# Kernel optimization log

Measured on AMD Instinct MI355X. Metric: run time of the kernel, lower is better.

Reference implementation:

```python
import jax, jax.numpy as jnp
import numpy as np
from jax import lax

DN = ('NCHW', 'OIHW', 'NCHW')


def setup_inputs() -> dict:
    key = jax.random.key(0)
    ks = jax.random.split(key, 5)
    B, C, H, W = 1, 128, 64, 64
    heads = 4
    return {
        'x_q': jax.random.normal(ks[0], (B, C, H, W), jnp.float32),
        'x_kv': jax.random.normal(ks[1], (B, C, H, W), jnp.float32),
        'w_qkv': jax.random.normal(ks[2], (3 * C, C, 1, 1), jnp.float32) * 0.05,
        'w_dw': jax.random.normal(ks[3], (3 * C, 1, 3, 3), jnp.float32) * 0.2,
        'w_proj': jax.random.normal(ks[4], (C, C, 1, 1), jnp.float32) * 0.05,
        'temperature': jnp.ones((heads, 1, 1), jnp.float32),
    }


def reference(x_q, x_kv, w_qkv, w_dw, w_proj, temperature):
    B, C, H, W = x_q.shape
    heads = temperature.shape[0]
    hd = C // heads
    N = H * W

    # shared qkv 1x1 conv + depthwise 3x3 conv on concatenated [2B,C,H,W]
    x = jnp.concatenate([x_q, x_kv], axis=0)
    qkv = lax.conv_general_dilated(x, w_qkv, (1, 1), 'VALID', dimension_numbers=DN)
    qkv = lax.conv_general_dilated(qkv, w_dw, (1, 1), 'SAME',
                                   feature_group_count=3 * C, dimension_numbers=DN)
    q, k, v = jnp.split(qkv, 3, axis=1)
    q = q[:B]          # query branch from x_q
    k = k[B:]          # key/value branch from x_kv
    v = v[B:]

    def to_heads(t):   # [B,C,H,W] -> [B,h,N,d]
        return t.reshape(B, heads, hd, N).transpose(0, 1, 3, 2)

    attn = jnp.einsum('bhnd,bhmd->bhnm', to_heads(q), to_heads(k)) * temperature
    attn = jax.nn.softmax(attn, axis=-1)
    out = jnp.einsum('bhnm,bhmd->bhnd', attn, to_heads(v))
    out = out.transpose(0, 1, 3, 2).reshape(B, C, H, W)
    return lax.conv_general_dilated(out, w_proj, (1, 1), 'VALID', dimension_numbers=DN)
```

## Files before the change

### kernel.cpp

```cpp
#include <hip/hip_runtime.h>

typedef short bf16x4 __attribute__((ext_vector_type(4)));
typedef short bf16x8 __attribute__((ext_vector_type(8)));
typedef float f32x4 __attribute__((ext_vector_type(4)));
typedef unsigned short u16x4 __attribute__((ext_vector_type(4)));
typedef unsigned short u16x8 __attribute__((ext_vector_type(8)));

__device__ __forceinline__ unsigned short f2bf(float f) {
  union { float f; unsigned u; } v; v.f = f;
  unsigned r = v.u + 0x7FFFu + ((v.u >> 16) & 1u);
  return (unsigned short)(r >> 16);
}
__device__ __forceinline__ unsigned fbits(float f) {
  union { float f; unsigned u; } x; x.f = f; return x.u;
}
__device__ __forceinline__ float bfloat(unsigned u) {
  union { unsigned u; float f; } x; x.u = u; return x.f;
}
__device__ __forceinline__ float fexp2(float x) {
#if __has_builtin(__builtin_amdgcn_exp2f)
  return __builtin_amdgcn_exp2f(x);
#else
  return exp2f(x);
#endif
}
__device__ __forceinline__ f32x4 pv_mfma(bf16x4 a, bf16x4 b, f32x4 c) {
#if __has_builtin(__builtin_amdgcn_mfma_f32_16x16x16bf16_1k)
  return __builtin_amdgcn_mfma_f32_16x16x16bf16_1k(a, b, c, 0, 0, 0);
#else
  bf16x8 az = {a[0], a[1], a[2], a[3], 0, 0, 0, 0};
  bf16x8 bz = {b[0], b[1], b[2], b[3], 0, 0, 0, 0};
  return __builtin_amdgcn_mfma_f32_16x16x32_bf16(az, bz, c, 0, 0, 0);
#endif
}

__global__ __launch_bounds__(256)
void cast_kernel(const float* __restrict__ Xq, const float* __restrict__ Xkv,
                 const float* __restrict__ Wqkv, const float* __restrict__ Wproj,
                 unsigned short* __restrict__ XT, unsigned short* __restrict__ Wq16,
                 unsigned short* __restrict__ Wph, unsigned short* __restrict__ Wpl)
{
  const int b = blockIdx.x, t = threadIdx.x;
  if (b < 256) {
    __shared__ __align__(16) float Tl[64][68];
    const int img = b >> 7, kt = (b >> 6) & 1, nt = b & 63;
    const float* X = img ? Xkv : Xq;
    #pragma unroll
    for (int i = 0; i < 4; ++i) {
      int e = i * 256 + t;
      int r = e >> 4, c4 = (e & 15) * 4;
      *(f32x4*)&Tl[r][c4] = *(const f32x4*)&X[(kt * 64 + r) * 4096 + nt * 64 + c4];
    }
    __syncthreads();
    unsigned short* out = XT + img * (4096 * 128);
    #pragma unroll
    for (int i = 0; i < 2; ++i) {
      int u = i * 256 + t;
      int n = u >> 3, kg = u & 7;
      u16x8 tv;
      #pragma unroll
      for (int j = 0; j < 8; ++j) tv[j] = f2bf(Tl[kg * 8 + j][n]);
      *(u16x8*)&out[(nt * 64 + n) * 128 + kt * 64 + kg * 8] = tv;
    }
  } else {
    const int wb = b - 256;
    if (wb < 3) {
      #pragma unroll 4
      for (int i = 0; i < 64; ++i) {
        int idx = wb * 16384 + i * 256 + t;
        Wq16[idx] = f2bf(Wqkv[idx]);
      }
    } else {
      #pragma unroll 4
      for (int i = 0; i < 64; ++i) {
        int idx = i * 256 + t;
        float v = Wproj[idx];
        unsigned short h = f2bf(v);
        float hf = bfloat((unsigned)h << 16);
        Wph[idx] = h;
        Wpl[idx] = f2bf(v - hf);
      }
    }
  }
}

__global__ __launch_bounds__(256)
void gemm_qkv_kernel(const unsigned short* __restrict__ XT,
                     const unsigned short* __restrict__ Wq16,
                     unsigned short* __restrict__ Y16)
{
  const int t = threadIdx.x;
  const int w = t >> 6, c = t & 15, g = (t & 63) >> 4;
  const int n0 = blockIdx.x * 32;
  const int ob = blockIdx.y;
  const int o_base = ob * 64 + w * 16;
  const unsigned short* B = XT + (ob >= 2 ? 4096 * 128 : 0);
  f32x4 acc0 = {0.f, 0.f, 0.f, 0.f}, acc1 = {0.f, 0.f, 0.f, 0.f};
  #pragma unroll
  for (int ks = 0; ks < 4; ++ks) {
    bf16x8 a = *(const bf16x8*)&Wq16[(o_base + c) * 128 + ks * 32 + g * 8];
    bf16x8 b0 = *(const bf16x8*)&B[(n0 + c) * 128 + ks * 32 + g * 8];
    bf16x8 b1 = *(const bf16x8*)&B[(n0 + 16 + c) * 128 + ks * 32 + g * 8];
    acc0 = __builtin_amdgcn_mfma_f32_16x16x32_bf16(a, b0, acc0, 0, 0, 0);
    acc1 = __builtin_amdgcn_mfma_f32_16x16x32_bf16(a, b1, acc1, 0, 0, 0);
  }
  #pragma unroll
  for (int i = 0; i < 4; ++i) {
    Y16[(o_base + 4 * g + i) * 4096 + n0 + c] = f2bf(acc0[i]);
    Y16[(o_base + 4 * g + i) * 4096 + n0 + 16 + c] = f2bf(acc1[i]);
  }
}

__global__ __launch_bounds__(256)
void gemm_proj_kernel(const unsigned short* __restrict__ Oth,
                      const unsigned short* __restrict__ Otl,
                      const unsigned short* __restrict__ Wph,
                      const unsigned short* __restrict__ Wpl, float* __restrict__ Y)
{
  const int t = threadIdx.x;
  const int w = t >> 6, c = t & 15, g = (t & 63) >> 4;
  const int n0 = blockIdx.x * 32;
  const int o_base = blockIdx.y * 64 + w * 16;
  f32x4 acc0 = {0.f, 0.f, 0.f, 0.f}, acc1 = {0.f, 0.f, 0.f, 0.f};
  #pragma unroll
  for (int ks = 0; ks < 4; ++ks) {
    const int ko = ks * 32 + g * 8;
    bf16x8 ah = *(const bf16x8*)&Wph[(o_base + c) * 128 + ko];
    bf16x8 al = *(const bf16x8*)&Wpl[(o_base + c) * 128 + ko];
    bf16x8 bh0 = *(const bf16x8*)&Oth[(n0 + c) * 128 + ko];
    bf16x8 bl0 = *(const bf16x8*)&Otl[(n0 + c) * 128 + ko];
    bf16x8 bh1 = *(const bf16x8*)&Oth[(n0 + 16 + c) * 128 + ko];
    bf16x8 bl1 = *(const bf16x8*)&Otl[(n0 + 16 + c) * 128 + ko];
    acc0 = __builtin_amdgcn_mfma_f32_16x16x32_bf16(al, bh0, acc0, 0, 0, 0);
    acc0 = __builtin_amdgcn_mfma_f32_16x16x32_bf16(ah, bl0, acc0, 0, 0, 0);
    acc0 = __builtin_amdgcn_mfma_f32_16x16x32_bf16(ah, bh0, acc0, 0, 0, 0);
    acc1 = __builtin_amdgcn_mfma_f32_16x16x32_bf16(al, bh1, acc1, 0, 0, 0);
    acc1 = __builtin_amdgcn_mfma_f32_16x16x32_bf16(ah, bl1, acc1, 0, 0, 0);
    acc1 = __builtin_amdgcn_mfma_f32_16x16x32_bf16(ah, bh1, acc1, 0, 0, 0);
  }
  #pragma unroll
  for (int i = 0; i < 4; ++i) {
    Y[(o_base + 4 * g + i) * 4096 + n0 + c] = acc0[i];
    Y[(o_base + 4 * g + i) * 4096 + n0 + 16 + c] = acc1[i];
  }
}

__global__ __launch_bounds__(256)
void dwconv_kernel(const unsigned short* __restrict__ T16, const float* __restrict__ Wd,
                   const float* __restrict__ temp, unsigned short* __restrict__ Qb)
{
  __shared__ __align__(16) float P[4096];
  const int jc = blockIdx.x;
  const int t = threadIdx.x;
  const unsigned short* in = T16 + jc * 4096;
  #pragma unroll
  for (int i = 0; i < 2; ++i) {
    u16x8 v = *(const u16x8*)&in[(i * 256 + t) * 8];
    #pragma unroll
    for (int j = 0; j < 8; ++j)
      P[(i * 256 + t) * 8 + j] = bfloat((unsigned)v[j] << 16);
  }
  float w[9];
  #pragma unroll
  for (int k = 0; k < 9; ++k) w[k] = Wd[jc * 9 + k];
  const float scale = (jc < 128) ? temp[jc >> 5] * 1.4426950408889634f : 1.0f;
  __syncthreads();
  unsigned short* out = Qb + jc * 4096;
  #pragma unroll 4
  for (int i = 0; i < 16; ++i) {
    int idx = i * 256 + t;
    int y = idx >> 6, x = idx & 63;
    float acc = 0.f;
    #pragma unroll
    for (int dy = -1; dy <= 1; ++dy) {
      int yy = y + dy;
      if (yy < 0 || yy > 63) continue;
      #pragma unroll
      for (int dx = -1; dx <= 1; ++dx) {
        int xx = x + dx;
        if (xx < 0 || xx > 63) continue;
        acc += w[(dy + 1) * 3 + (dx + 1)] * P[yy * 64 + xx];
      }
    }
    out[idx] = f2bf(acc * scale);
  }
}

#define KOFF (128 * 4096)
#define VOFF (256 * 4096)

__global__ __launch_bounds__(1024, 4)
void attn_kernel(const unsigned short* __restrict__ Qb,
                 unsigned short* __restrict__ Oth, unsigned short* __restrict__ Otl)
{
  __shared__ __align__(16) char lds[40960];
  const int t = threadIdx.x;
  const int wv = t >> 6;
  const int g4 = wv >> 2, qw = wv & 3;
  const int l = t & 63;
  const int c = l & 15, g = l >> 4;
  const int h = blockIdx.y;
  const int nq = blockIdx.x * 64;
  const int m0w = wv * 256;

  bf16x8 qf[4];
  #pragma unroll
  for (int s = 0; s < 4; ++s)
    #pragma unroll
    for (int e = 0; e < 8; ++e)
      qf[s][e] = (short)Qb[(h * 32 + g * 8 + e) * 4096 + nq + s * 16 + c];

  f32x4 oh[4][2];
  #pragma unroll
  for (int s = 0; s < 4; ++s) {
    oh[s][0] = (f32x4){0.f, 0.f, 0.f, 0.f};
    oh[s][1] = (f32x4){0.f, 0.f, 0.f, 0.f};
  }
  float lsum[4] = {0.f, 0.f, 0.f, 0.f};

  const unsigned short* Kb = Qb + KOFF + (h * 32 + g * 8) * 4096 + m0w + c;
  const unsigned short* Vb0 = Qb + VOFF + (h * 32 + c) * 4096 + m0w + g * 4;
  const unsigned short* Vb1 = Vb0 + 16 * 4096;

  #pragma unroll 4
  for (int j = 0; j < 16; ++j) {
    bf16x8 kf;
    #pragma unroll
    for (int e = 0; e < 8; ++e)
      kf[e] = (short)Kb[e * 4096 + j * 16];
    bf16x4 vf0 = *(const bf16x4*)&Vb0[j * 16];
    bf16x4 vf1 = *(const bf16x4*)&Vb1[j * 16];
    #pragma unroll
    for (int s = 0; s < 4; ++s) {
      f32x4 z = {0.f, 0.f, 0.f, 0.f};
      f32x4 sv = __builtin_amdgcn_mfma_f32_16x16x32_bf16(kf, qf[s], z, 0, 0, 0);
      unsigned u0 = fbits(fexp2(sv[0]));
      unsigned u1 = fbits(fexp2(sv[1]));
      unsigned u2 = fbits(fexp2(sv[2]));
      unsigned u3 = fbits(fexp2(sv[3]));
      unsigned t0 = u0 & 0xFFFF0000u, t1 = u1 & 0xFFFF0000u;
      unsigned t2 = u2 & 0xFFFF0000u, t3 = u3 & 0xFFFF0000u;
      lsum[s] += (bfloat(t0) + bfloat(t1)) + (bfloat(t2) + bfloat(t3));
      union { unsigned u[2]; bf16x4 v; } pu;
      pu.u[0] = __builtin_amdgcn_perm(u1, u0, 0x07060302);
      pu.u[1] = __builtin_amdgcn_perm(u3, u2, 0x07060302);
      oh[s][0] = pv_mfma(vf0, pu.v, oh[s][0]);
      oh[s][1] = pv_mfma(vf1, pu.v, oh[s][1]);
    }
  }

  #pragma unroll
  for (int s = 0; s < 4; ++s) {
    lsum[s] += __shfl_xor(lsum[s], 16, 64);
    lsum[s] += __shfl_xor(lsum[s], 32, 64);
  }

  __syncthreads();
  float* OG  = (float*)lds;
  float* lfq = (float*)(lds + 34048);
  float* lf  = (float*)(lds + 36864);
  if (l < 16) {
    #pragma unroll
    for (int s = 0; s < 4; ++s)
      lf[(g4 * 4 + qw) * 64 + s * 16 + c] = lsum[s];
  }
  for (int r = 0; r < 4; ++r) {
    if (qw == r) {
      #pragma unroll
      for (int s = 0; s < 4; ++s)
        #pragma unroll
        for (int i = 0; i < 4; ++i) {
          int d0 = 4 * g + i;
          float* p0 = &OG[g4 * 2112 + d0 * 66 + s * 16 + c];
          float* p1 = &OG[g4 * 2112 + (16 + d0) * 66 + s * 16 + c];
          if (r == 0) { *p0 = oh[s][0][i];  *p1 = oh[s][1][i]; }
          else        { *p0 += oh[s][0][i]; *p1 += oh[s][1][i]; }
        }
    }
    __syncthreads();
  }
  if (t < 64) {
    float a = 0.f;
    #pragma unroll
    for (int ww = 0; ww < 16; ++ww) a += lf[ww * 64 + t];
    lfq[t] = a;
  }
  __syncthreads();

  #pragma unroll
  for (int e = t; e < 2048; e += 1024) {
    int d = e & 31, q = e >> 5;
    float s4 = OG[0 * 2112 + d * 66 + q] + OG[1 * 2112 + d * 66 + q] +
               OG[2 * 2112 + d * 66 + q] + OG[3 * 2112 + d * 66 + q];
    float val = s4 / lfq[q];
    unsigned short hi = f2bf(val);
    float hf = bfloat((unsigned)hi << 16);
    int idx = (blockIdx.x * 64 + q) * 128 + h * 32 + d;
    Oth[idx] = hi;
    Otl[idx] = f2bf(val - hf);
  }
}

extern "C" void kernel_launch(void* const* d_in, const int* in_sizes, int n_in,
                              void* d_out, int out_size, void* d_ws, size_t ws_size,
                              hipStream_t stream) {
  const float* xq    = (const float*)d_in[0];
  const float* xkv   = (const float*)d_in[1];
  const float* wqkv  = (const float*)d_in[2];
  const float* wdw   = (const float*)d_in[3];
  const float* wproj = (const float*)d_in[4];
  const float* temp  = (const float*)d_in[5];
  float* out = (float*)d_out;

  char* ws = (char*)d_ws;
  unsigned short* t16  = (unsigned short*)ws;
  unsigned short* qb   = (unsigned short*)(ws + 3145728);
  unsigned short* xt   = (unsigned short*)(ws + 6291456);
  unsigned short* wq16 = (unsigned short*)(ws + 8388608);
  unsigned short* wph  = (unsigned short*)(ws + 8486912);
  unsigned short* wpl  = (unsigned short*)(ws + 8519680);
  unsigned short* oth  = (unsigned short*)(ws + 8552448);
  unsigned short* otl  = (unsigned short*)(ws + 9601024);

  cast_kernel<<<dim3(260), 256, 0, stream>>>(xq, xkv, wqkv, wproj, xt, wq16, wph, wpl);
  gemm_qkv_kernel<<<dim3(128, 6), 256, 0, stream>>>(xt, wq16, t16);
  dwconv_kernel<<<dim3(384), 256, 0, stream>>>(t16, wdw, temp, qb);
  attn_kernel<<<dim3(64, 4), 1024, 0, stream>>>(qb, oth, otl);
  gemm_proj_kernel<<<dim3(128, 2), 256, 0, stream>>>(oth, otl, wph, wpl, out);
}
```

Measured before the change: 57.39 us.

## Store Q and K token-major so attention loads fragments as vectors

The depthwise conv kernel now writes Q and K transposed to a [head][token][dim] layout and V separately, so the attention kernel can fetch each bf16x8 Q/K fragment with one 16-byte load instead of eight strided 2-byte gathers. The aim is to cut global load instruction count and uncoalesced traffic in the attention inner loop. In exchange, the conv kernel's Q/K stores become strided by 32 elements, which costs write coalescing there. Separately, the softmax denominator now sums the full-precision exp values instead of bf16-truncated ones, removing a few masking ops but making the sum slightly inconsistent with the bf16 P used in the PV product.

```diff
diff --git a/kernel.cpp b/kernel.cpp
--- a/kernel.cpp
+++ b/kernel.cpp
@@ -147,7 +147,8 @@
 
 __global__ __launch_bounds__(256)
 void dwconv_kernel(const unsigned short* __restrict__ T16, const float* __restrict__ Wd,
-                   const float* __restrict__ temp, unsigned short* __restrict__ Qb)
+                   const float* __restrict__ temp, unsigned short* __restrict__ Qt,
+                   unsigned short* __restrict__ Kt, unsigned short* __restrict__ Vb)
 {
   __shared__ __align__(16) float P[4096];
   const int jc = blockIdx.x;
@@ -165,7 +166,12 @@
   for (int k = 0; k < 9; ++k) w[k] = Wd[jc * 9 + k];
   const float scale = (jc < 128) ? temp[jc >> 5] * 1.4426950408889634f : 1.0f;
   __syncthreads();
-  unsigned short* out = Qb + jc * 4096;
+
+  const int hh = (jc >> 5) & 3, dd = jc & 31;
+  unsigned short* outT = (jc < 128 ? Qt : Kt) + (hh * 4096) * 32 + dd;
+  unsigned short* outV = Vb + (jc - 256) * 4096;
+  const bool is_v = (jc >= 256);
+
   #pragma unroll 4
   for (int i = 0; i < 16; ++i) {
     int idx = i * 256 + t;
@@ -182,15 +188,16 @@
         acc += w[(dy + 1) * 3 + (dx + 1)] * P[yy * 64 + xx];
       }
     }
-    out[idx] = f2bf(acc * scale);
-  }
-}
-
-#define KOFF (128 * 4096)
-#define VOFF (256 * 4096)
+    unsigned short r = f2bf(acc * scale);
+    if (is_v) outV[idx] = r;
+    else      outT[idx * 32] = r;
+  }
+}
 
 __global__ __launch_bounds__(1024, 4)
-void attn_kernel(const unsigned short* __restrict__ Qb,
+void attn_kernel(const unsigned short* __restrict__ Qt,
+                 const unsigned short* __restrict__ Kt,
+                 const unsigned short* __restrict__ Vb,
                  unsigned short* __restrict__ Oth, unsigned short* __restrict__ Otl)
 {
   __shared__ __align__(16) char lds[40960];
@@ -206,9 +213,7 @@
   bf16x8 qf[4];
   #pragma unroll
   for (int s = 0; s < 4; ++s)
-    #pragma unroll
-    for (int e = 0; e < 8; ++e)
-      qf[s][e] = (short)Qb[(h * 32 + g * 8 + e) * 4096 + nq + s * 16 + c];
+    qf[s] = *(const bf16x8*)&Qt[(h * 4096 + nq + s * 16 + c) * 32 + g * 8];
 
   f32x4 oh[4][2];
   #pragma unroll
@@ -218,32 +223,27 @@
   }
   float lsum[4] = {0.f, 0.f, 0.f, 0.f};
 
-  const unsigned short* Kb = Qb + KOFF + (h * 32 + g * 8) * 4096 + m0w + c;
-  const unsigned short* Vb0 = Qb + VOFF + (h * 32 + c) * 4096 + m0w + g * 4;
+  const unsigned short* Kb  = Kt + (h * 4096 + m0w + c) * 32 + g * 8;
+  const unsigned short* Vb0 = Vb + (h * 32 + c) * 4096 + m0w + g * 4;
   const unsigned short* Vb1 = Vb0 + 16 * 4096;
 
   #pragma unroll 4
   for (int j = 0; j < 16; ++j) {
-    bf16x8 kf;
-    #pragma unroll
-    for (int e = 0; e < 8; ++e)
-      kf[e] = (short)Kb[e * 4096 + j * 16];
+    bf16x8 kf = *(const bf16x8*)&Kb[j * 512];
     bf16x4 vf0 = *(const bf16x4*)&Vb0[j * 16];
     bf16x4 vf1 = *(const bf16x4*)&Vb1[j * 16];
     #pragma unroll
     for (int s = 0; s < 4; ++s) {
       f32x4 z = {0.f, 0.f, 0.f, 0.f};
       f32x4 sv = __builtin_amdgcn_mfma_f32_16x16x32_bf16(kf, qf[s], z, 0, 0, 0);
-      unsigned u0 = fbits(fexp2(sv[0]));
-      unsigned u1 = fbits(fexp2(sv[1]));
-      unsigned u2 = fbits(fexp2(sv[2]));
-      unsigned u3 = fbits(fexp2(sv[3]));
-      unsigned t0 = u0 & 0xFFFF0000u, t1 = u1 & 0xFFFF0000u;
-      unsigned t2 = u2 & 0xFFFF0000u, t3 = u3 & 0xFFFF0000u;
-      lsum[s] += (bfloat(t0) + bfloat(t1)) + (bfloat(t2) + bfloat(t3));
+      float e0 = fexp2(sv[0]);
+      float e1 = fexp2(sv[1]);
+      float e2 = fexp2(sv[2]);
+      float e3 = fexp2(sv[3]);
+      lsum[s] += (e0 + e1) + (e2 + e3);
       union { unsigned u[2]; bf16x4 v; } pu;
-      pu.u[0] = __builtin_amdgcn_perm(u1, u0, 0x07060302);
-      pu.u[1] = __builtin_amdgcn_perm(u3, u2, 0x07060302);
+      pu.u[0] = __builtin_amdgcn_perm(fbits(e1), fbits(e0), 0x07060302);
+      pu.u[1] = __builtin_amdgcn_perm(fbits(e3), fbits(e2), 0x07060302);
       oh[s][0] = pv_mfma(vf0, pu.v, oh[s][0]);
       oh[s][1] = pv_mfma(vf1, pu.v, oh[s][1]);
     }
@@ -314,17 +314,19 @@
 
   char* ws = (char*)d_ws;
   unsigned short* t16  = (unsigned short*)ws;
-  unsigned short* qb   = (unsigned short*)(ws + 3145728);
-  unsigned short* xt   = (unsigned short*)(ws + 6291456);
-  unsigned short* wq16 = (unsigned short*)(ws + 8388608);
-  unsigned short* wph  = (unsigned short*)(ws + 8486912);
-  unsigned short* wpl  = (unsigned short*)(ws + 8519680);
+  unsigned short* xt   = (unsigned short*)(ws + 3145728);
+  unsigned short* wq16 = (unsigned short*)(ws + 5242880);
+  unsigned short* wph  = (unsigned short*)(ws + 5341184);
+  unsigned short* wpl  = (unsigned short*)(ws + 5373952);
+  unsigned short* qt   = (unsigned short*)(ws + 5406720);
+  unsigned short* kt   = (unsigned short*)(ws + 6455296);
+  unsigned short* vb   = (unsigned short*)(ws + 7503872);
   unsigned short* oth  = (unsigned short*)(ws + 8552448);
   unsigned short* otl  = (unsigned short*)(ws + 9601024);
 
   cast_kernel<<<dim3(260), 256, 0, stream>>>(xq, xkv, wqkv, wproj, xt, wq16, wph, wpl);
   gemm_qkv_kernel<<<dim3(128, 6), 256, 0, stream>>>(xt, wq16, t16);
-  dwconv_kernel<<<dim3(384), 256, 0, stream>>>(t16, wdw, temp, qb);
-  attn_kernel<<<dim3(64, 4), 1024, 0, stream>>>(qb, oth, otl);
+  dwconv_kernel<<<dim3(384), 256, 0, stream>>>(t16, wdw, temp, qt, kt, vb);
+  attn_kernel<<<dim3(64, 4), 1024, 0, stream>>>(qt, kt, vb, oth, otl);
   gemm_proj_kernel<<<dim3(128, 2), 256, 0, stream>>>(oth, otl, wph, wpl, out);
 }
```

After: 57.38 us. No clear change (-0.0%).
